# Kernel tuning notes

Hardware: AMD Instinct MI355X
Metric: run time of the kernel (lower is better)

## Reference

```python
import jax, jax.numpy as jnp
import numpy as np

DIAG = 64          # dynamic_mask_scale: |i-j| >= DIAG is masked
NEG_INF = float('-inf')

def _band_mask(L, diagonal):
    # True where masked out: j >= i + diagonal or i >= j + diagonal  <=>  |i-j| >= diagonal
    i = jnp.arange(L)[:, None]
    j = jnp.arange(L)[None, :]
    return jnp.abs(i - j) >= diagonal  # [L, L] bool

def setup_inputs() -> dict:
    key = jax.random.key(0)
    k1, k2, k3, k4 = jax.random.split(key, 4)
    B, L, H, E = 2, 2048, 8, 64
    queries = jax.random.normal(k1, (B, L, H, E), dtype=jnp.float32)
    keys = jax.random.normal(k2, (B, L, H, E), dtype=jnp.float32)
    values = jax.random.normal(k3, (B, L, H, E), dtype=jnp.float32)
    sigma = jax.random.normal(k4, (B, L, H), dtype=jnp.float32)
    attn_mask = jnp.zeros((B, 1, L, L), dtype=bool)  # unused (dynamic mask path)
    return {"queries": queries, "keys": keys, "values": values,
            "sigma": sigma, "attn_mask": attn_mask}

def reference(queries, keys, values, sigma, attn_mask):
    B, L, H, E = queries.shape
    scale = 1.0 / jnp.sqrt(jnp.float32(E))
    # scores: [B, H, L, S]
    scores = jnp.einsum('blhe,bshe->bhls', queries, keys)
    mask = _band_mask(L, DIAG)  # [L, L]
    scores = jnp.where(mask[None, None, :, :], NEG_INF, scores)
    attn = scale * scores
    series = jax.nn.softmax(attn, axis=-1)  # dropout p=0 -> identity
    V = jnp.einsum('bhls,bshd->blhd', series, values)
    return (V, series)
```

## Files before the change

kernel.cpp:

```cpp
#include <hip/hip_runtime.h>
#include <cstdint>

#define BB    2
#define LL    2048
#define HH    8
#define EE    64
#define DIAG  64
#define RR    16
#define WCAP  144
#define SKB   36
#define PS    148
#define NT    256

__global__ __launch_bounds__(NT, 4) void anomaly_attn_kernel(
    const float* __restrict__ Q,
    const float* __restrict__ K,
    const float* __restrict__ V,
    float* __restrict__ outV,
    float* __restrict__ outS)
{
    __shared__ unsigned lds_kv[WCAP * SKB];
    __shared__ float    lds_q[RR * EE];
    __shared__ float    lds_sp[RR * PS];

    const int bid  = blockIdx.x;
    const int gblk = (bid & 7) * 256 + (bid >> 3);
    const int rb   = gblk & 127;
    const int h    = (gblk >> 7) & 7;
    const int b    = gblk >> 10;
    const int i0   = rb * RR;

    const int t    = threadIdx.x;
    const int wave = t >> 6;
    const int lane = t & 63;

    const size_t headOff = ((size_t)b * LL * HH + h) * EE;
    const int    rowStr  = HH * EE;

    const int j0  = i0 - 64;
    const int j04 = j0 >> 2;

    auto pack2 = [](float x, float y) -> unsigned {
        unsigned ux = __float_as_uint(x);
        unsigned uy = __float_as_uint(y);
        unsigned bx = (ux + 0x7FFFu + ((ux >> 16) & 1u)) >> 16;
        unsigned by = (uy + 0x7FFFu + ((uy >> 16) & 1u)) >> 16;
        return bx | (by << 16);
    };
    auto lo = [](unsigned u) -> float { return __uint_as_float(u << 16); };
    auto hi = [](unsigned u) -> float { return __uint_as_float(u & 0xFFFF0000u); };

    {
        const float4 z4 = make_float4(0.f, 0.f, 0.f, 0.f);
        float4* zp = (float4*)(lds_sp + wave * 4 * PS);
        for (int z = lane; z < PS; z += 64) zp[z] = z4;
    }

    {
        const int qrow = t >> 4, qf = t & 15;
        *(float4*)(lds_q + qrow * EE + qf * 4) =
            *(const float4*)(Q + headOff + (size_t)(i0 + qrow) * rowStr + qf * 4);
        for (int idx = t; idx < WCAP * 16; idx += NT) {
            const int trow = idx >> 4, tf = idx & 15;
            int j = j0 + trow; j = j < 0 ? 0 : (j > LL - 1 ? LL - 1 : j);
            const float4 kv = *(const float4*)(K + headOff + (size_t)j * rowStr + tf * 4);
            uint2 pk; pk.x = pack2(kv.x, kv.y); pk.y = pack2(kv.z, kv.w);
            *(uint2*)(lds_kv + trow * SKB + tf * 2) = pk;
        }
    }
    __syncthreads();

    const float scale = 0.125f;
#pragma unroll
    for (int p = 0; p < 2; ++p) {
        const int rA = wave * 4 + 2 * p;
        const int rB = rA + 1;
        const int jrelA = rA + 1 + lane;
        const int jrelB = rA + 65 + lane;
        const unsigned* k1 = lds_kv + jrelA * SKB;
        const unsigned* k2 = lds_kv + jrelB * SKB;
        const float* qA = lds_q + rA * EE;
        const float* qB = lds_q + rB * EE;
        float sA1 = 0.f, sA2 = 0.f, sB1 = 0.f, sB2 = 0.f;
#pragma unroll
        for (int c = 0; c < 8; ++c) {
            const uint4 a4 = *(const uint4*)(k1 + c * 4);
            const uint4 b4 = *(const uint4*)(k2 + c * 4);
            const float4 qa0 = *(const float4*)(qA + c * 8);
            const float4 qa1 = *(const float4*)(qA + c * 8 + 4);
            const float4 qb0 = *(const float4*)(qB + c * 8);
            const float4 qb1 = *(const float4*)(qB + c * 8 + 4);
            const float a0 = lo(a4.x), a1 = hi(a4.x), a2 = lo(a4.y), a3 = hi(a4.y);
            const float a4f = lo(a4.z), a5 = hi(a4.z), a6 = lo(a4.w), a7 = hi(a4.w);
            const float b0 = lo(b4.x), b1 = hi(b4.x), b2 = lo(b4.y), b3 = hi(b4.y);
            const float b4f = lo(b4.z), b5 = hi(b4.z), b6 = lo(b4.w), b7 = hi(b4.w);
            sA1 += qa0.x*a0 + qa0.y*a1 + qa0.z*a2 + qa0.w*a3
                 + qa1.x*a4f + qa1.y*a5 + qa1.z*a6 + qa1.w*a7;
            sA2 += qa0.x*b0 + qa0.y*b1 + qa0.z*b2 + qa0.w*b3
                 + qa1.x*b4f + qa1.y*b5 + qa1.z*b6 + qa1.w*b7;
            sB1 += qb0.x*a0 + qb0.y*a1 + qb0.z*a2 + qb0.w*a3
                 + qb1.x*a4f + qb1.y*a5 + qb1.z*a6 + qb1.w*a7;
            sB2 += qb0.x*b0 + qb0.y*b1 + qb0.z*b2 + qb0.w*b3
                 + qb1.x*b4f + qb1.y*b5 + qb1.z*b6 + qb1.w*b7;
        }
        const int jA = j0 + jrelA;
        const int jB = j0 + jrelB;
        const bool vA1 = (jA >= 0);
        const bool vA2 = (lane <= 62) && (jB < LL);
        const bool vB1 = (lane >= 1) && (jA >= 0);
        const bool vB2 = (jB < LL);
        float eA1 = vA1 ? sA1 * scale : -3.0e38f;
        float eA2 = vA2 ? sA2 * scale : -3.0e38f;
        float eB1 = vB1 ? sB1 * scale : -3.0e38f;
        float eB2 = vB2 ? sB2 * scale : -3.0e38f;

        float mA = fmaxf(eA1, eA2);
        float mB = fmaxf(eB1, eB2);
#pragma unroll
        for (int off = 1; off < 64; off <<= 1) {
            mA = fmaxf(mA, __shfl_xor(mA, off, 64));
            mB = fmaxf(mB, __shfl_xor(mB, off, 64));
        }
        float pA1 = vA1 ? __expf(eA1 - mA) : 0.f;
        float pA2 = vA2 ? __expf(eA2 - mA) : 0.f;
        float pB1 = vB1 ? __expf(eB1 - mB) : 0.f;
        float pB2 = vB2 ? __expf(eB2 - mB) : 0.f;
        float lA = pA1 + pA2;
        float lB = pB1 + pB2;
#pragma unroll
        for (int off = 1; off < 64; off <<= 1) {
            lA += __shfl_xor(lA, off, 64);
            lB += __shfl_xor(lB, off, 64);
        }
        const float invA = 1.0f / lA;
        const float invB = 1.0f / lB;
        lds_sp[rA * PS + jrelA] = pA1 * invA;
        lds_sp[rA * PS + jrelB] = pA2 * invA;
        lds_sp[rB * PS + jrelA] = pB1 * invB;
        lds_sp[rB * PS + jrelB] = pB2 * invB;
    }
    __syncthreads();

    for (int idx = t; idx < WCAP * 16; idx += NT) {
        const int trow = idx >> 4, tf = idx & 15;
        int j = j0 + trow; j = j < 0 ? 0 : (j > LL - 1 ? LL - 1 : j);
        const float4 vv = *(const float4*)(V + headOff + (size_t)j * rowStr + tf * 4);
        uint2 pk; pk.x = pack2(vv.x, vv.y); pk.y = pack2(vv.z, vv.w);
        *(uint2*)(lds_kv + trow * SKB + tf * 2) = pk;
    }
    __syncthreads();

    {
        const int wstart4 = j04 < 0 ? 0 : j04;
        int wend4 = j04 + 36; if (wend4 > LL / 4) wend4 = LL / 4;
        for (int r4 = 0; r4 < 4; ++r4) {
            const int r = wave * 4 + r4;
            const int i = i0 + r;
            float4* srow4 = (float4*)(outS + (((size_t)(b * HH + h)) * LL + i) * LL);
            const float4* sp4 = (const float4*)(lds_sp + r * PS);
#pragma unroll
            for (int k = 0; k < 8; ++k) {
                const int col4 = lane + k * 64;
                float4 v = make_float4(0.f, 0.f, 0.f, 0.f);
                if (col4 >= wstart4 && col4 < wend4)
                    v = sp4[col4 - j04];
                srow4[col4] = v;
            }
        }
    }

    {
        const int e4   = lane & 15;
        const int jsub = lane >> 4;
        const int rr0  = wave * 4;
        const float* pbase = lds_sp + rr0 * PS;
        float4 a0 = make_float4(0,0,0,0), a1 = a0, a2 = a0, a3 = a0;
#pragma unroll
        for (int k = 0; k < WCAP / 4; ++k) {
            const int jrel = jsub + 4 * k;
            const uint2 pv = *(const uint2*)(lds_kv + jrel * SKB + e4 * 2);
            const float v0 = lo(pv.x), v1 = hi(pv.x), v2 = lo(pv.y), v3 = hi(pv.y);
            const float w0 = pbase[jrel];
            const float w1 = pbase[PS + jrel];
            const float w2 = pbase[2 * PS + jrel];
            const float w3 = pbase[3 * PS + jrel];
            a0.x += w0 * v0; a0.y += w0 * v1; a0.z += w0 * v2; a0.w += w0 * v3;
            a1.x += w1 * v0; a1.y += w1 * v1; a1.z += w1 * v2; a1.w += w1 * v3;
            a2.x += w2 * v0; a2.y += w2 * v1; a2.z += w2 * v2; a2.w += w2 * v3;
            a3.x += w3 * v0; a3.y += w3 * v1; a3.z += w3 * v2; a3.w += w3 * v3;
        }
#pragma unroll
        for (int off = 16; off <= 32; off <<= 1) {
            a0.x += __shfl_xor(a0.x, off, 64); a0.y += __shfl_xor(a0.y, off, 64);
            a0.z += __shfl_xor(a0.z, off, 64); a0.w += __shfl_xor(a0.w, off, 64);
            a1.x += __shfl_xor(a1.x, off, 64); a1.y += __shfl_xor(a1.y, off, 64);
            a1.z += __shfl_xor(a1.z, off, 64); a1.w += __shfl_xor(a1.w, off, 64);
            a2.x += __shfl_xor(a2.x, off, 64); a2.y += __shfl_xor(a2.y, off, 64);
            a2.z += __shfl_xor(a2.z, off, 64); a2.w += __shfl_xor(a2.w, off, 64);
            a3.x += __shfl_xor(a3.x, off, 64); a3.y += __shfl_xor(a3.y, off, 64);
            a3.z += __shfl_xor(a3.z, off, 64); a3.w += __shfl_xor(a3.w, off, 64);
        }
        if (lane < 16) {
            float4* o0 = (float4*)(outV + headOff + (size_t)(i0 + rr0 + 0) * rowStr);
            float4* o1 = (float4*)(outV + headOff + (size_t)(i0 + rr0 + 1) * rowStr);
            float4* o2 = (float4*)(outV + headOff + (size_t)(i0 + rr0 + 2) * rowStr);
            float4* o3 = (float4*)(outV + headOff + (size_t)(i0 + rr0 + 3) * rowStr);
            o0[e4] = a0; o1[e4] = a1; o2[e4] = a2; o3[e4] = a3;
        }
    }
}

extern "C" void kernel_launch(void* const* d_in, const int* in_sizes, int n_in,
                              void* d_out, int out_size, void* d_ws, size_t ws_size,
                              hipStream_t stream) {
    const float* Q = (const float*)d_in[0];
    const float* K = (const float*)d_in[1];
    const float* V = (const float*)d_in[2];

    float* outV = (float*)d_out;
    float* outS = (float*)d_out + (size_t)BB * LL * HH * EE;

    const int grid = (BB * HH * LL) / RR;
    anomaly_attn_kernel<<<grid, NT, 0, stream>>>(Q, K, V, outV, outS);
}
```

Before: 337.7 us.

## Load K and V together into separate LDS buffers and stream series rows directly

K and V tiles now go into separate LDS buffers, both loaded up front, which removes a barrier pair and the serial V reload after softmax. Each wave writes its own two rows of the series output right after computing them, as scalar stores for the band and float4 zero stores elsewhere, so the large zero-fill overlaps with compute from other waves. LDS row stride and the occupancy hint are adjusted to fit the extra buffer, trading possible occupancy for fewer barriers. The band writes are now unaligned scalar stores instead of float4 stores.

```diff
diff --git a/kernel.cpp b/kernel.cpp
--- a/kernel.cpp
+++ b/kernel.cpp
@@ -8,18 +8,19 @@
 #define DIAG  64
 #define RR    16
 #define WCAP  144
-#define SKB   36
+#define SKB   34
 #define PS    148
 #define NT    256
 
-__global__ __launch_bounds__(NT, 4) void anomaly_attn_kernel(
+__global__ __launch_bounds__(NT, 3) void anomaly_attn_kernel(
     const float* __restrict__ Q,
     const float* __restrict__ K,
     const float* __restrict__ V,
     float* __restrict__ outV,
     float* __restrict__ outS)
 {
-    __shared__ unsigned lds_kv[WCAP * SKB];
+    __shared__ unsigned lds_k[WCAP * SKB];
+    __shared__ unsigned lds_v[WCAP * SKB];
     __shared__ float    lds_q[RR * EE];
     __shared__ float    lds_sp[RR * PS];
 
@@ -39,6 +40,10 @@
 
     const int j0  = i0 - 64;
     const int j04 = j0 >> 2;
+    const int wstart4 = j04 < 0 ? 0 : j04;
+    int wend4 = j04 + 36; if (wend4 > LL / 4) wend4 = LL / 4;
+    const int wwid4  = wend4 - wstart4;
+    const int nzero4 = LL / 4 - wwid4;
 
     auto pack2 = [](float x, float y) -> unsigned {
         unsigned ux = __float_as_uint(x);
@@ -65,7 +70,14 @@
             int j = j0 + trow; j = j < 0 ? 0 : (j > LL - 1 ? LL - 1 : j);
             const float4 kv = *(const float4*)(K + headOff + (size_t)j * rowStr + tf * 4);
             uint2 pk; pk.x = pack2(kv.x, kv.y); pk.y = pack2(kv.z, kv.w);
-            *(uint2*)(lds_kv + trow * SKB + tf * 2) = pk;
+            *(uint2*)(lds_k + trow * SKB + tf * 2) = pk;
+        }
+        for (int idx = t; idx < WCAP * 16; idx += NT) {
+            const int trow = idx >> 4, tf = idx & 15;
+            int j = j0 + trow; j = j < 0 ? 0 : (j > LL - 1 ? LL - 1 : j);
+            const float4 vv = *(const float4*)(V + headOff + (size_t)j * rowStr + tf * 4);
+            uint2 pk; pk.x = pack2(vv.x, vv.y); pk.y = pack2(vv.z, vv.w);
+            *(uint2*)(lds_v + trow * SKB + tf * 2) = pk;
         }
     }
     __syncthreads();
@@ -77,8 +89,8 @@
         const int rB = rA + 1;
         const int jrelA = rA + 1 + lane;
         const int jrelB = rA + 65 + lane;
-        const unsigned* k1 = lds_kv + jrelA * SKB;
-        const unsigned* k2 = lds_kv + jrelB * SKB;
+        const unsigned* k1 = lds_k + jrelA * SKB;
+        const unsigned* k2 = lds_k + jrelB * SKB;
         const float* qA = lds_q + rA * EE;
         const float* qB = lds_q + rB * EE;
         float sA1 = 0.f, sA2 = 0.f, sB1 = 0.f, sB2 = 0.f;
@@ -138,33 +150,26 @@
         lds_sp[rA * PS + jrelB] = pA2 * invA;
         lds_sp[rB * PS + jrelA] = pB1 * invB;
         lds_sp[rB * PS + jrelB] = pB2 * invB;
-    }
-    __syncthreads();
-
-    for (int idx = t; idx < WCAP * 16; idx += NT) {
-        const int trow = idx >> 4, tf = idx & 15;
-        int j = j0 + trow; j = j < 0 ? 0 : (j > LL - 1 ? LL - 1 : j);
-        const float4 vv = *(const float4*)(V + headOff + (size_t)j * rowStr + tf * 4);
-        uint2 pk; pk.x = pack2(vv.x, vv.y); pk.y = pack2(vv.z, vv.w);
-        *(uint2*)(lds_kv + trow * SKB + tf * 2) = pk;
-    }
-    __syncthreads();
-
-    {
-        const int wstart4 = j04 < 0 ? 0 : j04;
-        int wend4 = j04 + 36; if (wend4 > LL / 4) wend4 = LL / 4;
-        for (int r4 = 0; r4 < 4; ++r4) {
-            const int r = wave * 4 + r4;
+
+#pragma unroll
+        for (int rs = 0; rs < 2; ++rs) {
+            const int r = rA + rs;
             const int i = i0 + r;
-            float4* srow4 = (float4*)(outS + (((size_t)(b * HH + h)) * LL + i) * LL);
-            const float4* sp4 = (const float4*)(lds_sp + r * PS);
-#pragma unroll
-            for (int k = 0; k < 8; ++k) {
-                const int col4 = lane + k * 64;
-                float4 v = make_float4(0.f, 0.f, 0.f, 0.f);
-                if (col4 >= wstart4 && col4 < wend4)
-                    v = sp4[col4 - j04];
-                srow4[col4] = v;
+            float* srow = outS + (((size_t)(b * HH + h)) * LL + i) * LL;
+            const float* sp = lds_sp + r * PS;
+            const int c0 = j0 + lane;
+            if ((unsigned)c0 < (unsigned)LL) srow[c0] = sp[lane];
+            const int c1 = j0 + 64 + lane;
+            if ((unsigned)c1 < (unsigned)LL) srow[c1] = sp[64 + lane];
+            if (lane < 16) {
+                const int c2 = j0 + 128 + lane;
+                if ((unsigned)c2 < (unsigned)LL) srow[c2] = sp[128 + lane];
+            }
+            float4* srow4 = (float4*)srow;
+            const float4 z = make_float4(0.f, 0.f, 0.f, 0.f);
+            for (int c = lane; c < nzero4; c += 64) {
+                const int col4 = c < wstart4 ? c : c + wwid4;
+                srow4[col4] = z;
             }
         }
     }
@@ -178,7 +183,7 @@
 #pragma unroll
         for (int k = 0; k < WCAP / 4; ++k) {
             const int jrel = jsub + 4 * k;
-            const uint2 pv = *(const uint2*)(lds_kv + jrel * SKB + e4 * 2);
+            const uint2 pv = *(const uint2*)(lds_v + jrel * SKB + e4 * 2);
             const float v0 = lo(pv.x), v1 = hi(pv.x), v2 = lo(pv.y), v3 = hi(pv.y);
             const float w0 = pbase[jrel];
             const float w1 = pbase[PS + jrel];
```

New measurement: 348.2 us. +3.1%, slower.

## Compute banded QK scores with bf16 MFMA and reorder barriers around softmax

Applied to the files above, without the earlier changes.

Replaces the per-lane scalar FMA dot products for the banded Q·K scores with bf16 MFMA 16x16x32 instructions over the 16x144 tile, with Q now packed to bf16 in LDS. Softmax is then applied row by row over the full 144-wide window held in LDS. One barrier is removed by overlapping the V load with the outS write, since each wave only touches its own rows. This cuts ALU work in the score phase, but Q is now rounded to bf16, which costs some accuracy.

```diff
diff --git a/kernel.cpp b/kernel.cpp
--- a/kernel.cpp
+++ b/kernel.cpp
@@ -9,8 +9,12 @@
 #define RR    16
 #define WCAP  144
 #define SKB   36
-#define PS    148
+#define SQB   36
+#define PS    160
 #define NT    256
+
+typedef __attribute__((ext_vector_type(8))) short bf16x8;
+typedef __attribute__((ext_vector_type(4))) float f32x4;
 
 __global__ __launch_bounds__(NT, 4) void anomaly_attn_kernel(
     const float* __restrict__ Q,
@@ -19,8 +23,8 @@
     float* __restrict__ outV,
     float* __restrict__ outS)
 {
-    __shared__ unsigned lds_kv[WCAP * SKB];
-    __shared__ float    lds_q[RR * EE];
+    __shared__ unsigned lds_k[WCAP * SKB];
+    __shared__ unsigned lds_qb[RR * SQB];
     __shared__ float    lds_sp[RR * PS];
 
     const int bid  = blockIdx.x;
@@ -39,6 +43,8 @@
 
     const int j0  = i0 - 64;
     const int j04 = j0 >> 2;
+
+    float* srow0 = outS + (((size_t)(b * HH + h)) * LL + i0) * LL;
 
     auto pack2 = [](float x, float y) -> unsigned {
         unsigned ux = __float_as_uint(x);
@@ -51,112 +57,86 @@
     auto hi = [](unsigned u) -> float { return __uint_as_float(u & 0xFFFF0000u); };
 
     {
-        const float4 z4 = make_float4(0.f, 0.f, 0.f, 0.f);
-        float4* zp = (float4*)(lds_sp + wave * 4 * PS);
-        for (int z = lane; z < PS; z += 64) zp[z] = z4;
-    }
-
-    {
         const int qrow = t >> 4, qf = t & 15;
-        *(float4*)(lds_q + qrow * EE + qf * 4) =
-            *(const float4*)(Q + headOff + (size_t)(i0 + qrow) * rowStr + qf * 4);
+        const float4 qv = *(const float4*)(Q + headOff + (size_t)(i0 + qrow) * rowStr + qf * 4);
+        uint2 qp; qp.x = pack2(qv.x, qv.y); qp.y = pack2(qv.z, qv.w);
+        *(uint2*)(lds_qb + qrow * SQB + qf * 2) = qp;
         for (int idx = t; idx < WCAP * 16; idx += NT) {
             const int trow = idx >> 4, tf = idx & 15;
             int j = j0 + trow; j = j < 0 ? 0 : (j > LL - 1 ? LL - 1 : j);
             const float4 kv = *(const float4*)(K + headOff + (size_t)j * rowStr + tf * 4);
             uint2 pk; pk.x = pack2(kv.x, kv.y); pk.y = pack2(kv.z, kv.w);
-            *(uint2*)(lds_kv + trow * SKB + tf * 2) = pk;
+            *(uint2*)(lds_k + trow * SKB + tf * 2) = pk;
         }
     }
     __syncthreads();
 
+    {
+        const int quad = lane >> 4;
+        const int l16  = lane & 15;
+        const bf16x8 a0 = *(const bf16x8*)(lds_qb + l16 * SQB + quad * 4);
+        const bf16x8 a1 = *(const bf16x8*)(lds_qb + l16 * SQB + quad * 4 + 16);
+        for (int n = wave; n < 9; n += 4) {
+            const unsigned* kb = lds_k + (16 * n + l16) * SKB + quad * 4;
+            const bf16x8 b0 = *(const bf16x8*)(kb);
+            const bf16x8 b1 = *(const bf16x8*)(kb + 16);
+            f32x4 acc = {0.f, 0.f, 0.f, 0.f};
+            acc = __builtin_amdgcn_mfma_f32_16x16x32_bf16(a0, b0, acc, 0, 0, 0);
+            acc = __builtin_amdgcn_mfma_f32_16x16x32_bf16(a1, b1, acc, 0, 0, 0);
+            float* dst = lds_sp + (quad * 4) * PS + 16 * n + l16;
+            dst[0 * PS] = acc[0];
+            dst[1 * PS] = acc[1];
+            dst[2 * PS] = acc[2];
+            dst[3 * PS] = acc[3];
+        }
+    }
+    __syncthreads();
+
     const float scale = 0.125f;
-#pragma unroll
-    for (int p = 0; p < 2; ++p) {
-        const int rA = wave * 4 + 2 * p;
-        const int rB = rA + 1;
-        const int jrelA = rA + 1 + lane;
-        const int jrelB = rA + 65 + lane;
-        const unsigned* k1 = lds_kv + jrelA * SKB;
-        const unsigned* k2 = lds_kv + jrelB * SKB;
-        const float* qA = lds_q + rA * EE;
-        const float* qB = lds_q + rB * EE;
-        float sA1 = 0.f, sA2 = 0.f, sB1 = 0.f, sB2 = 0.f;
-#pragma unroll
-        for (int c = 0; c < 8; ++c) {
-            const uint4 a4 = *(const uint4*)(k1 + c * 4);
-            const uint4 b4 = *(const uint4*)(k2 + c * 4);
-            const float4 qa0 = *(const float4*)(qA + c * 8);
-            const float4 qa1 = *(const float4*)(qA + c * 8 + 4);
-            const float4 qb0 = *(const float4*)(qB + c * 8);
-            const float4 qb1 = *(const float4*)(qB + c * 8 + 4);
-            const float a0 = lo(a4.x), a1 = hi(a4.x), a2 = lo(a4.y), a3 = hi(a4.y);
-            const float a4f = lo(a4.z), a5 = hi(a4.z), a6 = lo(a4.w), a7 = hi(a4.w);
-            const float b0 = lo(b4.x), b1 = hi(b4.x), b2 = lo(b4.y), b3 = hi(b4.y);
-            const float b4f = lo(b4.z), b5 = hi(b4.z), b6 = lo(b4.w), b7 = hi(b4.w);
-            sA1 += qa0.x*a0 + qa0.y*a1 + qa0.z*a2 + qa0.w*a3
-                 + qa1.x*a4f + qa1.y*a5 + qa1.z*a6 + qa1.w*a7;
-            sA2 += qa0.x*b0 + qa0.y*b1 + qa0.z*b2 + qa0.w*b3
-                 + qa1.x*b4f + qa1.y*b5 + qa1.z*b6 + qa1.w*b7;
-            sB1 += qb0.x*a0 + qb0.y*a1 + qb0.z*a2 + qb0.w*a3
-                 + qb1.x*a4f + qb1.y*a5 + qb1.z*a6 + qb1.w*a7;
-            sB2 += qb0.x*b0 + qb0.y*b1 + qb0.z*b2 + qb0.w*b3
-                 + qb1.x*b4f + qb1.y*b5 + qb1.z*b6 + qb1.w*b7;
-        }
-        const int jA = j0 + jrelA;
-        const int jB = j0 + jrelB;
-        const bool vA1 = (jA >= 0);
-        const bool vA2 = (lane <= 62) && (jB < LL);
-        const bool vB1 = (lane >= 1) && (jA >= 0);
-        const bool vB2 = (jB < LL);
-        float eA1 = vA1 ? sA1 * scale : -3.0e38f;
-        float eA2 = vA2 ? sA2 * scale : -3.0e38f;
-        float eB1 = vB1 ? sB1 * scale : -3.0e38f;
-        float eB2 = vB2 ? sB2 * scale : -3.0e38f;
-
-        float mA = fmaxf(eA1, eA2);
-        float mB = fmaxf(eB1, eB2);
-#pragma unroll
-        for (int off = 1; off < 64; off <<= 1) {
-            mA = fmaxf(mA, __shfl_xor(mA, off, 64));
-            mB = fmaxf(mB, __shfl_xor(mB, off, 64));
-        }
-        float pA1 = vA1 ? __expf(eA1 - mA) : 0.f;
-        float pA2 = vA2 ? __expf(eA2 - mA) : 0.f;
-        float pB1 = vB1 ? __expf(eB1 - mB) : 0.f;
-        float pB2 = vB2 ? __expf(eB2 - mB) : 0.f;
-        float lA = pA1 + pA2;
-        float lB = pB1 + pB2;
-#pragma unroll
-        for (int off = 1; off < 64; off <<= 1) {
-            lA += __shfl_xor(lA, off, 64);
-            lB += __shfl_xor(lB, off, 64);
-        }
-        const float invA = 1.0f / lA;
-        const float invB = 1.0f / lB;
-        lds_sp[rA * PS + jrelA] = pA1 * invA;
-        lds_sp[rA * PS + jrelB] = pA2 * invA;
-        lds_sp[rB * PS + jrelA] = pB1 * invB;
-        lds_sp[rB * PS + jrelB] = pB2 * invB;
-    }
-    __syncthreads();
+    for (int r4 = 0; r4 < 4; ++r4) {
+        const int r = wave * 4 + r4;
+        float* sp = lds_sp + r * PS;
+        const float x1 = sp[lane];
+        const float x2 = sp[64 + lane];
+        const float x3 = (lane < 16) ? sp[128 + lane] : 0.f;
+        const bool v1 = (lane >= r + 1) && (j0 + lane >= 0);
+        const bool v2 = (i0 + lane < LL);
+        const bool v3 = (lane < 16) && (lane <= r - 1) && (i0 + 64 + lane < LL);
+        float e1 = v1 ? x1 * scale : -3.0e38f;
+        float e2 = v2 ? x2 * scale : -3.0e38f;
+        float e3 = v3 ? x3 * scale : -3.0e38f;
+
+        float m = fmaxf(e1, fmaxf(e2, e3));
+#pragma unroll
+        for (int off = 1; off < 64; off <<= 1)
+            m = fmaxf(m, __shfl_xor(m, off, 64));
+        float p1 = v1 ? __expf(e1 - m) : 0.f;
+        float p2 = v2 ? __expf(e2 - m) : 0.f;
+        float p3 = v3 ? __expf(e3 - m) : 0.f;
+        float l = p1 + p2 + p3;
+#pragma unroll
+        for (int off = 1; off < 64; off <<= 1)
+            l += __shfl_xor(l, off, 64);
+        const float inv = 1.0f / l;
+        sp[lane]      = p1 * inv;
+        sp[64 + lane] = p2 * inv;
+        if (lane < 16) sp[128 + lane] = p3 * inv;
+    }
 
     for (int idx = t; idx < WCAP * 16; idx += NT) {
         const int trow = idx >> 4, tf = idx & 15;
         int j = j0 + trow; j = j < 0 ? 0 : (j > LL - 1 ? LL - 1 : j);
         const float4 vv = *(const float4*)(V + headOff + (size_t)j * rowStr + tf * 4);
         uint2 pk; pk.x = pack2(vv.x, vv.y); pk.y = pack2(vv.z, vv.w);
-        *(uint2*)(lds_kv + trow * SKB + tf * 2) = pk;
-    }
-    __syncthreads();
+        *(uint2*)(lds_k + trow * SKB + tf * 2) = pk;
+    }
 
     {
         const int wstart4 = j04 < 0 ? 0 : j04;
         int wend4 = j04 + 36; if (wend4 > LL / 4) wend4 = LL / 4;
         for (int r4 = 0; r4 < 4; ++r4) {
             const int r = wave * 4 + r4;
-            const int i = i0 + r;
-            float4* srow4 = (float4*)(outS + (((size_t)(b * HH + h)) * LL + i) * LL);
+            float4* srow4 = (float4*)(srow0 + (size_t)r * LL);
             const float4* sp4 = (const float4*)(lds_sp + r * PS);
 #pragma unroll
             for (int k = 0; k < 8; ++k) {
@@ -168,6 +148,7 @@
             }
         }
     }
+    __syncthreads();
 
     {
         const int e4   = lane & 15;
@@ -178,7 +159,7 @@
 #pragma unroll
         for (int k = 0; k < WCAP / 4; ++k) {
             const int jrel = jsub + 4 * k;
-            const uint2 pv = *(const uint2*)(lds_kv + jrel * SKB + e4 * 2);
+            const uint2 pv = *(const uint2*)(lds_k + jrel * SKB + e4 * 2);
             const float v0 = lo(pv.x), v1 = hi(pv.x), v2 = lo(pv.y), v3 = hi(pv.y);
             const float w0 = pbase[jrel];
             const float w1 = pbase[PS + jrel];
```

Result: no change. 331.7 us (-1.8%).
